# Kernel optimization log

Hardware: AMD Instinct MI355X
Metric: run time of the kernel (lower is better)

## Reference

```python
import jax, jax.numpy as jnp
import numpy as np

N = 50000
E = 1600000

def setup_inputs() -> dict:
    key = jax.random.key(0)
    ks = jax.random.split(key, 8)
    x = jax.random.normal(ks[0], (N, 512), dtype=jnp.float32)
    edge_index = jax.random.randint(ks[1], (2, E), 0, N, dtype=jnp.int32).astype(jnp.int64)
    eigenvectors = jax.random.normal(ks[2], (N, 128), dtype=jnp.float32)
    W1 = jax.random.normal(ks[3], (512, 128), dtype=jnp.float32) * 0.04
    b1 = jnp.zeros((128,), dtype=jnp.float32)
    W2 = jax.random.normal(ks[4], (128, 64), dtype=jnp.float32) * 0.09
    b2 = jnp.zeros((64,), dtype=jnp.float32)
    lin_W = jax.random.normal(ks[5], (128, 64), dtype=jnp.float32) * 0.09
    W3 = jax.random.normal(ks[6], (128, 40), dtype=jnp.float32) * 0.09
    b3 = jnp.zeros((40,), dtype=jnp.float32)
    return {"x": x, "edge_index": edge_index, "eigenvectors": eigenvectors,
            "W1": W1, "b1": b1, "W2": W2, "b2": b2, "lin_W": lin_W, "W3": W3, "b3": b3}

def _gcn_norm(edge_index, num_nodes):
    # add self loops, then symmetric normalization D^-1/2 (A+I) D^-1/2
    loop = jnp.arange(num_nodes, dtype=edge_index.dtype)
    row = jnp.concatenate([edge_index[0], loop])  # source
    col = jnp.concatenate([edge_index[1], loop])  # target
    w = jnp.ones(row.shape[0], dtype=jnp.float32)
    deg = jax.ops.segment_sum(w, col, num_segments=num_nodes)
    dis = jnp.where(deg > 0, 1.0 / jnp.sqrt(deg), 0.0)
    norm = dis[row] * dis[col]  # [E+N]
    return row, col, norm

def _gcn_conv(h, W, b, row, col, norm, num_nodes):
    h = h @ W                                  # [N, d_out] linear first (PyG order)
    msg = h[row] * norm[:, None]               # gather + scale, [E+N, d_out]
    out = jax.ops.segment_sum(msg, col, num_segments=num_nodes)  # scatter-add
    return out + b

def reference(x, edge_index, eigenvectors, W1, b1, W2, b2, lin_W, W3, b3):
    num_nodes = x.shape[0]
    row, col, norm = _gcn_norm(edge_index, num_nodes)
    h = jax.nn.relu(_gcn_conv(x, W1, b1, row, col, norm, num_nodes))
    # dropout omitted: eval mode (deterministic reference)
    h = jax.nn.relu(_gcn_conv(h, W2, b2, row, col, norm, num_nodes))
    xp = eigenvectors @ lin_W                  # Linear(spec_in, spec_out, bias=False)
    h = jnp.concatenate([h, xp], axis=1)       # [N, h2+spec_out]
    h = _gcn_conv(h, W3, b3, row, col, norm, num_nodes)
    return jax.nn.log_softmax(h, axis=1)
```

## Files before the change

### kernel.cpp

```cpp
#include <hip/hip_runtime.h>
#include <cstdint>
#include <cstddef>

constexpr int BLK = 256;
constexpr int NB = 128;

static inline size_t ws_align(size_t x) { return (x + 255) & ~size_t(255); }

typedef __attribute__((ext_vector_type(8))) short bf16x8;
typedef __attribute__((ext_vector_type(4))) float f32x4;

__device__ inline unsigned short f2bf(float f) {
  unsigned int u = __float_as_uint(f);
  unsigned int r = (u + 0x7fffu + ((u >> 16) & 1u)) >> 16;
  return (unsigned short)r;
}
__device__ inline float bf2f(unsigned short u) {
  return __uint_as_float(((unsigned int)u) << 16);
}
__device__ inline float bf2f_lo(unsigned int w) {
  return __uint_as_float(w << 16);
}
__device__ inline float bf2f_hi(unsigned int w) {
  return __uint_as_float(w & 0xffff0000u);
}

__global__ void k_detect(const int* __restrict__ ei, int* __restrict__ flag) {
  int allz = 1;
  for (int i = 0; i < 32; ++i) allz &= (ei[2 * i + 1] == 0) ? 1 : 0;
  flag[0] = allz;
}

__global__ void k_pack_count(const int* __restrict__ ei, const int* __restrict__ flag,
                             unsigned int* __restrict__ pk,
                             int* __restrict__ cnt, int E, int nChunk) {
  __shared__ int hist[256];
  for (int t = threadIdx.x; t < 256; t += BLK) hist[t] = 0;
  __syncthreads();
  const bool i64 = flag[0] != 0;
  int beg = blockIdx.x * nChunk, end = min(beg + nChunk, E);
  for (int i = beg + threadIdx.x; i < end; i += BLK) {
    int row, col;
    if (i64) { row = ei[2 * i]; col = ei[2 * (E + i)]; }
    else     { row = ei[i];     col = ei[E + i]; }
    unsigned int p = ((unsigned int)col << 16) | (unsigned int)row;
    pk[i] = p;
    atomicAdd(&hist[col >> 8], 1);
  }
  __syncthreads();
  for (int t = threadIdx.x; t < 256; t += BLK) cnt[blockIdx.x * 256 + t] = hist[t];
}

__global__ void k_wscan(const int* __restrict__ cnt, int* __restrict__ woffs,
                        int* __restrict__ base, int nb, int E) {
  __shared__ int wsums[5];
  int w = threadIdx.x;
  int s = 0;
  for (int b = 0; b < nb; ++b) s += cnt[b * 256 + w];
  int lane = w & 63, wv = w >> 6;
  int x = s;
  #pragma unroll
  for (int sh = 1; sh < 64; sh <<= 1) { int t = __shfl_up(x, sh); if (lane >= sh) x += t; }
  if (lane == 63) wsums[wv] = x;
  __syncthreads();
  if (w == 0) { int a = 0; for (int k = 0; k < 4; ++k) { int t = wsums[k]; wsums[k] = a; a += t; } }
  __syncthreads();
  int excl = x - s + wsums[wv];
  woffs[w] = excl;
  if (w == 255) woffs[256] = excl + s;
  int start = excl;
  for (int b = 0; b < nb; ++b) { base[b * 256 + w] = start; start += cnt[b * 256 + w]; }
}

__global__ void k_part_scatter(const unsigned int* __restrict__ pk,
                               const int* __restrict__ base,
                               unsigned int* __restrict__ P, int E, int nChunk) {
  __shared__ int cur[256];
  for (int t = threadIdx.x; t < 256; t += BLK) cur[t] = base[blockIdx.x * 256 + t];
  __syncthreads();
  int beg = blockIdx.x * nChunk, end = min(beg + nChunk, E);
  for (int i = beg + threadIdx.x; i < end; i += BLK) {
    unsigned int p = pk[i];
    int pos = atomicAdd(&cur[p >> 24], 1);
    P[pos] = p;
  }
}

__global__ void k_window_build(const unsigned int* __restrict__ P,
                               const int* __restrict__ woffs,
                               float* __restrict__ dis, int* __restrict__ offs,
                               int* __restrict__ csr, int N, int E) {
  __shared__ int hist[256];
  __shared__ int wsums[5];
  __shared__ int lbase[256];
  const int node0 = blockIdx.x * 256;
  const int t = threadIdx.x;
  hist[t] = 0;
  __syncthreads();
  const int beg = woffs[blockIdx.x], end = woffs[blockIdx.x + 1];
  for (int i = beg + t; i < end; i += BLK)
    atomicAdd(&hist[(P[i] >> 16) & 255], 1);
  __syncthreads();
  const int dg = hist[t];
  if (node0 + t < N) dis[node0 + t] = 1.0f / sqrtf((float)(dg + 1));
  int lane = t & 63, wv = t >> 6;
  int x = dg;
  #pragma unroll
  for (int sh = 1; sh < 64; sh <<= 1) { int q = __shfl_up(x, sh); if (lane >= sh) x += q; }
  if (lane == 63) wsums[wv] = x;
  __syncthreads();
  if (t == 0) { int a = 0; for (int k = 0; k < 4; ++k) { int q = wsums[k]; wsums[k] = a; a += q; } }
  __syncthreads();
  const int goff = beg + (x - dg + wsums[wv]);
  if (node0 + t < N) offs[node0 + t] = goff;
  lbase[t] = goff;
  __syncthreads();
  for (int i = beg + t; i < end; i += BLK) {
    unsigned int p = P[i];
    int pos = atomicAdd(&lbase[(p >> 16) & 255], 1);
    csr[pos] = (int)(p & 0xffffu);
  }
  if (blockIdx.x == 0 && t == 0) offs[N] = E;
}

template<int K, int NOUT, int NOUTP>
__global__ void k_wt(const float* __restrict__ W, unsigned short* __restrict__ WT) {
  int i = blockIdx.x * BLK + threadIdx.x;
  if (i >= NOUTP * K) return;
  int n = i / K, k = i % K;
  float v = (n < NOUT) ? W[(size_t)k * NOUT + n] : 0.f;
  WT[i] = f2bf(v);
}

template<int K, int NT, int MR, bool AF32>
__launch_bounds__(256)
__global__ void k_mgemm(const void* __restrict__ Av, const unsigned short* __restrict__ WT,
                        const float* __restrict__ dis, unsigned short* __restrict__ C,
                        int ldc, int NOUT, int N) {
  const int tid = threadIdx.x;
  const int lane = tid & 63;
  const int wv = tid >> 6;
  const int m = lane & 15;
  const int kq = lane >> 4;
  const int orow = blockIdx.x * (64 * MR) + wv * (16 * MR);

  int rowc[MR];
  #pragma unroll
  for (int mr = 0; mr < MR; ++mr) {
    int row = orow + mr * 16 + m;
    rowc[mr] = row < N ? row : N - 1;
  }

  f32x4 acc[MR][NT];
  #pragma unroll
  for (int mr = 0; mr < MR; ++mr)
    #pragma unroll
    for (int t = 0; t < NT; ++t) acc[mr][t] = {0.f, 0.f, 0.f, 0.f};

  #pragma unroll 2
  for (int k0 = 0; k0 < K; k0 += 32) {
    bf16x8 af[MR];
    #pragma unroll
    for (int mr = 0; mr < MR; ++mr) {
      if constexpr (AF32) {
        const float* Arow = (const float*)Av + (size_t)rowc[mr] * K + kq * 8 + k0;
        float4 a0 = *(const float4*)Arow;
        float4 a1 = *(const float4*)(Arow + 4);
        af[mr][0] = (short)f2bf(a0.x); af[mr][1] = (short)f2bf(a0.y);
        af[mr][2] = (short)f2bf(a0.z); af[mr][3] = (short)f2bf(a0.w);
        af[mr][4] = (short)f2bf(a1.x); af[mr][5] = (short)f2bf(a1.y);
        af[mr][6] = (short)f2bf(a1.z); af[mr][7] = (short)f2bf(a1.w);
      } else {
        const unsigned short* Arow = (const unsigned short*)Av + (size_t)rowc[mr] * K + kq * 8 + k0;
        af[mr] = *(const bf16x8*)Arow;
      }
    }
    bf16x8 bf[NT];
    #pragma unroll
    for (int t = 0; t < NT; ++t)
      bf[t] = *(const bf16x8*)(WT + (size_t)(t * 16 + m) * K + k0 + kq * 8);
    #pragma unroll
    for (int t = 0; t < NT; ++t)
      #pragma unroll
      for (int mr = 0; mr < MR; ++mr)
        acc[mr][t] = __builtin_amdgcn_mfma_f32_16x16x32_bf16(af[mr], bf[t], acc[mr][t], 0, 0, 0);
  }
  #pragma unroll
  for (int mr = 0; mr < MR; ++mr) {
    #pragma unroll
    for (int r = 0; r < 4; ++r) {
      int rr = orow + mr * 16 + kq * 4 + r;
      if (rr < N) {
        float s = dis ? dis[rr] : 1.f;
        #pragma unroll
        for (int t = 0; t < NT; ++t) {
          int cc = t * 16 + m;
          if (cc < NOUT)
            C[(size_t)rr * ldc + cc] = f2bf(acc[mr][t][r] * s);
        }
      }
    }
  }
}

template<int D, bool RELU, bool LOGSM, bool OUTF32>
__launch_bounds__(BLK)
__global__ void k_agg(const unsigned short* __restrict__ g, int ldg,
                      const float* __restrict__ dis, const float* __restrict__ bias,
                      const int* __restrict__ offs, const int* __restrict__ csr,
                      void* __restrict__ dstv, int ldd, int N) {
  int wid = (blockIdx.x * BLK + threadIdx.x) >> 6;
  int lane = threadIdx.x & 63;
  if (wid >= N) return;
  float acc0 = 0.f, acc1 = 0.f;
  if constexpr (D == 128) {
    unsigned int w = *(const unsigned int*)&g[(size_t)wid * ldg + lane * 2];
    acc0 = bf2f_lo(w); acc1 = bf2f_hi(w);
  } else {
    if (lane < D) acc0 = bf2f(g[(size_t)wid * ldg + lane]);
  }
  int beg = offs[wid], end = offs[wid + 1];
  for (int e0 = beg; e0 < end; e0 += 64) {
    int cnt = end - e0; if (cnt > 64) cnt = 64;
    int u = (lane < cnt) ? csr[e0 + lane] : 0;
    int j = 0;
    for (; j + 3 < cnt; j += 4) {
      int u0 = __shfl(u, j), u1 = __shfl(u, j + 1);
      int u2 = __shfl(u, j + 2), u3 = __shfl(u, j + 3);
      if constexpr (D == 128) {
        unsigned int w0 = *(const unsigned int*)&g[(size_t)u0 * ldg + lane * 2];
        unsigned int w1 = *(const unsigned int*)&g[(size_t)u1 * ldg + lane * 2];
        unsigned int w2 = *(const unsigned int*)&g[(size_t)u2 * ldg + lane * 2];
        unsigned int w3 = *(const unsigned int*)&g[(size_t)u3 * ldg + lane * 2];
        acc0 += bf2f_lo(w0) + bf2f_lo(w1) + bf2f_lo(w2) + bf2f_lo(w3);
        acc1 += bf2f_hi(w0) + bf2f_hi(w1) + bf2f_hi(w2) + bf2f_hi(w3);
      } else {
        if (lane < D) {
          float v0 = bf2f(g[(size_t)u0 * ldg + lane]);
          float v1 = bf2f(g[(size_t)u1 * ldg + lane]);
          float v2 = bf2f(g[(size_t)u2 * ldg + lane]);
          float v3 = bf2f(g[(size_t)u3 * ldg + lane]);
          acc0 += (v0 + v1) + (v2 + v3);
        }
      }
    }
    for (; j < cnt; ++j) {
      int u0 = __shfl(u, j);
      if constexpr (D == 128) {
        unsigned int w0 = *(const unsigned int*)&g[(size_t)u0 * ldg + lane * 2];
        acc0 += bf2f_lo(w0); acc1 += bf2f_hi(w0);
      } else {
        if (lane < D) acc0 += bf2f(g[(size_t)u0 * ldg + lane]);
      }
    }
  }
  float dv = dis[wid];
  if constexpr (D == 128) {
    float ox = dv * acc0 + bias[lane * 2];
    float oy = dv * acc1 + bias[lane * 2 + 1];
    if constexpr (RELU) { ox = fmaxf(ox, 0.f); oy = fmaxf(oy, 0.f); }
    unsigned int pw = (unsigned int)f2bf(ox) | ((unsigned int)f2bf(oy) << 16);
    *(unsigned int*)&((unsigned short*)dstv)[(size_t)wid * ldd + lane * 2] = pw;
  } else {
    float o = 0.f;
    if (lane < D) o = dv * acc0 + bias[lane];
    if constexpr (RELU) o = fmaxf(o, 0.f);
    if constexpr (LOGSM) {
      float v = (lane < D) ? o : -__builtin_inff();
      float mx = v;
      #pragma unroll
      for (int s = 32; s >= 1; s >>= 1) mx = fmaxf(mx, __shfl_xor(mx, s));
      float ex = (lane < D) ? expf(v - mx) : 0.f;
      float sum = ex;
      #pragma unroll
      for (int s = 32; s >= 1; s >>= 1) sum += __shfl_xor(sum, s);
      o = v - mx - logf(sum);
    }
    if (lane < D) {
      if constexpr (OUTF32) ((float*)dstv)[(size_t)wid * ldd + lane] = o;
      else ((unsigned short*)dstv)[(size_t)wid * ldd + lane] = f2bf(o);
    }
  }
}

extern "C" void kernel_launch(void* const* d_in, const int* in_sizes, int n_in,
                              void* d_out, int out_size, void* d_ws, size_t ws_size,
                              hipStream_t stream) {
  const float* x    = (const float*)d_in[0];
  const int*   ei   = (const int*)d_in[1];
  const float* eig  = (const float*)d_in[2];
  const float* W1   = (const float*)d_in[3];
  const float* b1   = (const float*)d_in[4];
  const float* W2   = (const float*)d_in[5];
  const float* b2   = (const float*)d_in[6];
  const float* linW = (const float*)d_in[7];
  const float* W3   = (const float*)d_in[8];
  const float* b3   = (const float*)d_in[9];
  float* out = (float*)d_out;

  const int N = in_sizes[0] / 512;
  const int E = in_sizes[1] / 2;

  char* ws = (char*)d_ws;
  size_t off = 0;
  auto alloc = [&](size_t bytes) { char* p = ws + off; off = ws_align(off + bytes); return p; };
  unsigned int* pk = (unsigned int*)alloc((size_t)E * 4);
  unsigned int* P  = (unsigned int*)alloc((size_t)E * 4);
  int*   csr    = (int*)alloc((size_t)E * 4);
  int*   offs   = (int*)alloc((size_t)(N + 1) * 4);
  int*   cnt    = (int*)alloc((size_t)NB * 256 * 4);
  int*   base   = (int*)alloc((size_t)NB * 256 * 4);
  int*   woffs  = (int*)alloc(257 * 4);
  int*   flag   = (int*)alloc(256);
  float* dis    = (float*)alloc((size_t)N * 4);
  unsigned short* F = (unsigned short*)alloc((size_t)N * 128 * 2);
  unsigned short* G = (unsigned short*)alloc((size_t)N * 128 * 2);
  unsigned short* WT1 = (unsigned short*)alloc(128 * 512 * 2);
  unsigned short* WT2 = (unsigned short*)alloc(64 * 128 * 2);
  unsigned short* WTl = (unsigned short*)alloc(64 * 128 * 2);
  unsigned short* WT3 = (unsigned short*)alloc(48 * 128 * 2);

  const int nChunk = (E + NB - 1) / NB;
  const int NW = (N + 255) / 256;

  k_detect<<<1, 1, 0, stream>>>(ei, flag);
  k_pack_count<<<NB, BLK, 0, stream>>>(ei, flag, pk, cnt, E, nChunk);
  k_wscan<<<1, 256, 0, stream>>>(cnt, woffs, base, NB, E);
  k_part_scatter<<<NB, BLK, 0, stream>>>(pk, base, P, E, nChunk);
  k_window_build<<<NW, BLK, 0, stream>>>(P, woffs, dis, offs, csr, N, E);

  k_wt<512, 128, 128><<<(128 * 512 + BLK - 1) / BLK, BLK, 0, stream>>>(W1, WT1);
  k_wt<128, 64, 64><<<(64 * 128 + BLK - 1) / BLK, BLK, 0, stream>>>(W2, WT2);
  k_wt<128, 64, 64><<<(64 * 128 + BLK - 1) / BLK, BLK, 0, stream>>>(linW, WTl);
  k_wt<128, 40, 48><<<(48 * 128 + BLK - 1) / BLK, BLK, 0, stream>>>(W3, WT3);

  const int gG2 = (N + 127) / 128;
  const int gA = (N + 3) / 4;

  k_mgemm<512, 8, 2, true><<<gG2, BLK, 0, stream>>>(x, WT1, dis, F, 128, 128, N);
  k_agg<128, true, false, false><<<gA, BLK, 0, stream>>>(F, 128, dis, b1, offs, csr, G, 128, N);
  k_mgemm<128, 4, 2, false><<<gG2, BLK, 0, stream>>>(G, WT2, dis, F, 64, 64, N);
  k_mgemm<128, 4, 2, true><<<gG2, BLK, 0, stream>>>(eig, WTl, nullptr, G + 64, 128, 64, N);
  k_agg<64, true, false, false><<<gA, BLK, 0, stream>>>(F, 64, dis, b2, offs, csr, G, 128, N);
  k_mgemm<128, 3, 2, false><<<gG2, BLK, 0, stream>>>(G, WT3, dis, F, 40, 40, N);
  k_agg<40, false, true, true><<<gA, BLK, 0, stream>>>(F, 40, dis, b3, offs, csr, out, 40, N);
}
```

Baseline: 334.4 us.

## Add LDS double-buffered swizzled MFMA kernel for first-layer GEMM

```diff
diff --git a/kernel.cpp b/kernel.cpp
--- a/kernel.cpp
+++ b/kernel.cpp
@@ -130,6 +130,121 @@
   int n = i / K, k = i % K;
   float v = (n < NOUT) ? W[(size_t)k * NOUT + n] : 0.f;
   WT[i] = f2bf(v);
+}
+
+__global__ __launch_bounds__(256)
+void k_gemm1(const float* __restrict__ x, const unsigned short* __restrict__ WT,
+             const float* __restrict__ dis, unsigned short* __restrict__ C, int N) {
+  __shared__ unsigned short As[2][128 * 64];
+  __shared__ unsigned short Ws[2][128 * 64];
+  const int tid = threadIdx.x;
+  const int lane = tid & 63, wv = tid >> 6;
+  const int m = lane & 15, kq = lane >> 4;
+  const int row0 = blockIdx.x * 128;
+
+  const int srow = tid >> 1, shalf = tid & 1;
+  int sgrow = row0 + srow; if (sgrow >= N) sgrow = N - 1;
+  const float* xsrc = x + (size_t)sgrow * 512 + shalf * 32;
+  const unsigned short* wsrc = WT + (size_t)srow * 512 + shalf * 32;
+  int swoff[4];
+  #pragma unroll
+  for (int q = 0; q < 4; ++q)
+    swoff[q] = srow * 128 + ((shalf * 64 + q * 16) ^ ((srow & 7) << 4));
+
+  f32x4 acc[2][8];
+  #pragma unroll
+  for (int mr = 0; mr < 2; ++mr)
+    #pragma unroll
+    for (int t = 0; t < 8; ++t) acc[mr][t] = {0.f, 0.f, 0.f, 0.f};
+
+  float4 ar[8];
+  uint4  wr[4];
+
+  #pragma unroll
+  for (int q = 0; q < 8; ++q) ar[q] = *(const float4*)(xsrc + q * 4);
+  #pragma unroll
+  for (int q = 0; q < 4; ++q) wr[q] = *(const uint4*)(wsrc + q * 8);
+  {
+    char* Aw = (char*)As[0];
+    char* Ww = (char*)Ws[0];
+    #pragma unroll
+    for (int q = 0; q < 4; ++q) {
+      float4 a = ar[q * 2], b = ar[q * 2 + 1];
+      uint4 v;
+      v.x = (unsigned)f2bf(a.x) | ((unsigned)f2bf(a.y) << 16);
+      v.y = (unsigned)f2bf(a.z) | ((unsigned)f2bf(a.w) << 16);
+      v.z = (unsigned)f2bf(b.x) | ((unsigned)f2bf(b.y) << 16);
+      v.w = (unsigned)f2bf(b.z) | ((unsigned)f2bf(b.w) << 16);
+      *(uint4*)(Aw + swoff[q]) = v;
+      *(uint4*)(Ww + swoff[q]) = wr[q];
+    }
+  }
+  __syncthreads();
+
+  #pragma unroll 1
+  for (int i = 0; i < 8; ++i) {
+    const int p = i & 1;
+    if (i < 7) {
+      const float* xs = xsrc + (i + 1) * 64;
+      const unsigned short* wss = wsrc + (i + 1) * 64;
+      #pragma unroll
+      for (int q = 0; q < 8; ++q) ar[q] = *(const float4*)(xs + q * 4);
+      #pragma unroll
+      for (int q = 0; q < 4; ++q) wr[q] = *(const uint4*)(wss + q * 8);
+    }
+    const char* Ab = (const char*)As[p];
+    const char* Wb = (const char*)Ws[p];
+    #pragma unroll
+    for (int ks = 0; ks < 2; ++ks) {
+      bf16x8 af[2], bf[8];
+      #pragma unroll
+      for (int mr = 0; mr < 2; ++mr) {
+        int row = wv * 32 + mr * 16 + m;
+        int byte = row * 128 + (((ks * 64) + kq * 16) ^ ((row & 7) << 4));
+        af[mr] = *(const bf16x8*)(Ab + byte);
+      }
+      #pragma unroll
+      for (int t = 0; t < 8; ++t) {
+        int wrow = t * 16 + m;
+        int byte = wrow * 128 + (((ks * 64) + kq * 16) ^ ((wrow & 7) << 4));
+        bf[t] = *(const bf16x8*)(Wb + byte);
+      }
+      #pragma unroll
+      for (int t = 0; t < 8; ++t)
+        #pragma unroll
+        for (int mr = 0; mr < 2; ++mr)
+          acc[mr][t] = __builtin_amdgcn_mfma_f32_16x16x32_bf16(af[mr], bf[t], acc[mr][t], 0, 0, 0);
+    }
+    if (i < 7) {
+      char* Aw = (char*)As[p ^ 1];
+      char* Ww = (char*)Ws[p ^ 1];
+      #pragma unroll
+      for (int q = 0; q < 4; ++q) {
+        float4 a = ar[q * 2], b = ar[q * 2 + 1];
+        uint4 v;
+        v.x = (unsigned)f2bf(a.x) | ((unsigned)f2bf(a.y) << 16);
+        v.y = (unsigned)f2bf(a.z) | ((unsigned)f2bf(a.w) << 16);
+        v.z = (unsigned)f2bf(b.x) | ((unsigned)f2bf(b.y) << 16);
+        v.w = (unsigned)f2bf(b.z) | ((unsigned)f2bf(b.w) << 16);
+        *(uint4*)(Aw + swoff[q]) = v;
+        *(uint4*)(Ww + swoff[q]) = wr[q];
+      }
+      __syncthreads();
+    }
+  }
+
+  #pragma unroll
+  for (int mr = 0; mr < 2; ++mr)
+    #pragma unroll
+    for (int r = 0; r < 4; ++r) {
+      int rr = row0 + wv * 32 + mr * 16 + kq * 4 + r;
+      if (rr < N) {
+        float s = dis[rr];
+        #pragma unroll
+        for (int t = 0; t < 8; ++t)
+          C[(size_t)rr * 128 + t * 16 + m] = f2bf(acc[mr][t][r] * s);
+      }
+    }
 }
 
 template<int K, int NT, int MR, bool AF32>
@@ -157,7 +272,7 @@
     #pragma unroll
     for (int t = 0; t < NT; ++t) acc[mr][t] = {0.f, 0.f, 0.f, 0.f};
 
-  #pragma unroll 2
+  #pragma unroll 4
   for (int k0 = 0; k0 < K; k0 += 32) {
     bf16x8 af[MR];
     #pragma unroll
@@ -334,10 +449,11 @@
   k_wt<128, 64, 64><<<(64 * 128 + BLK - 1) / BLK, BLK, 0, stream>>>(linW, WTl);
   k_wt<128, 40, 48><<<(48 * 128 + BLK - 1) / BLK, BLK, 0, stream>>>(W3, WT3);
 
+  const int gG1 = (N + 127) / 128;
   const int gG2 = (N + 127) / 128;
   const int gA = (N + 3) / 4;
 
-  k_mgemm<512, 8, 2, true><<<gG2, BLK, 0, stream>>>(x, WT1, dis, F, 128, 128, N);
+  k_gemm1<<<gG1, BLK, 0, stream>>>(x, WT1, dis, F, N);
   k_agg<128, true, false, false><<<gA, BLK, 0, stream>>>(F, 128, dis, b1, offs, csr, G, 128, N);
   k_mgemm<128, 4, 2, false><<<gG2, BLK, 0, stream>>>(G, WT2, dis, F, 64, 64, N);
   k_mgemm<128, 4, 2, true><<<gG2, BLK, 0, stream>>>(eig, WTl, nullptr, G + 64, 128, 64, N);
```

New measurement: 321.8 us. 3.8% less time.
